# Optimization experiments

Hardware: AMD Instinct MI355X
Metric: run time of the kernel (lower is better)

## Reference

```python
import jax, jax.numpy as jnp
import numpy as np
import math

EMBED_DIM = 256
NUM_HEADS = 8
NUM_LEVELS = 4
NUM_POINTS_LIST = [4, 4, 4, 4]
SUM_P = sum(NUM_POINTS_LIST)            # 16
TOTAL_POINTS = NUM_HEADS * SUM_P        # 128
HEAD_DIM = EMBED_DIM // NUM_HEADS       # 32
OFFSET_SCALE = 0.5
SPATIAL = [(100, 100), (50, 50), (25, 25), (13, 13)]
BS, LQ = 16, 1000
LV = sum(h * w for h, w in SPATIAL)     # 13294
NUM_POINTS_SCALE = np.concatenate([np.full(n, 1.0 / n, np.float32) for n in NUM_POINTS_LIST])


def _grid_init_bias():
    # Faithful to MSDeformableAttention._reset_parameters
    thetas = np.arange(NUM_HEADS, dtype=np.float32) * (2.0 * math.pi / NUM_HEADS)
    grid = np.stack([np.cos(thetas), np.sin(thetas)], -1)          # [H,2]
    grid = grid / np.abs(grid).max(-1, keepdims=True)
    grid = np.tile(grid.reshape(NUM_HEADS, 1, 2), (1, SUM_P, 1))   # [H,SUM_P,2]
    scaling = np.concatenate([np.arange(1, n + 1) for n in NUM_POINTS_LIST]).reshape(1, -1, 1)
    grid = grid * scaling
    return grid.reshape(-1).astype(np.float32)                     # [TOTAL_POINTS*2]


def setup_inputs() -> dict:
    key = jax.random.key(0)
    k1, k2, k3, k4, k5 = jax.random.split(key, 5)
    return {
        "query": jax.random.normal(k1, (BS, LQ, EMBED_DIM), dtype=jnp.float32),
        "reference_points": jax.random.uniform(k2, (BS, LQ, 1, 4), dtype=jnp.float32),
        "value": jax.random.normal(k3, (BS, LV, EMBED_DIM), dtype=jnp.float32),
        "value_spatial_shapes": np.asarray(SPATIAL, dtype=np.int64),
        "W_off": jax.random.normal(k4, (EMBED_DIM, TOTAL_POINTS * 2), dtype=jnp.float32) * 0.01,
        "b_off": jnp.asarray(_grid_init_bias()),
        "W_attn": jax.random.normal(k5, (EMBED_DIM, TOTAL_POINTS), dtype=jnp.float32) * 0.01,
        "b_attn": jnp.zeros((TOTAL_POINTS,), dtype=jnp.float32),
    }


def _bilinear(valf, px, py, H, W):
    # valf: [bs, h, H*W, d]; px, py: [bs, h, n] pixel coords (grid_sample,
    # align_corners=False, padding_mode='zeros' semantics)
    x0 = jnp.floor(px)
    y0 = jnp.floor(py)
    wx1 = px - x0
    wy1 = py - y0
    x0i = x0.astype(jnp.int32)
    y0i = y0.astype(jnp.int32)

    def g(xi, yi):
        valid = ((xi >= 0) & (xi < W) & (yi >= 0) & (yi < H)).astype(valf.dtype)
        idx = jnp.clip(yi, 0, H - 1) * W + jnp.clip(xi, 0, W - 1)
        return jnp.take_along_axis(valf, idx[..., None], axis=2) * valid[..., None]

    return (g(x0i, y0i) * ((1 - wx1) * (1 - wy1))[..., None]
            + g(x0i + 1, y0i) * (wx1 * (1 - wy1))[..., None]
            + g(x0i, y0i + 1) * ((1 - wx1) * wy1)[..., None]
            + g(x0i + 1, y0i + 1) * (wx1 * wy1)[..., None])


def reference(query, reference_points, value, value_spatial_shapes, W_off, b_off, W_attn, b_attn):
    shapes = [(int(h), int(w)) for h, w in np.asarray(value_spatial_shapes)]
    bs, Lq, C = query.shape
    # sampling offsets + attention weights projections
    off = (query @ W_off + b_off).reshape(bs, Lq, NUM_HEADS, SUM_P, 2)
    attn = jax.nn.softmax((query @ W_attn + b_attn).reshape(bs, Lq, NUM_HEADS, SUM_P), axis=-1)
    nps = jnp.asarray(NUM_POINTS_SCALE)
    # reference_points: [bs,Lq,1,4] -> [:, :, None, :, :] broadcasts over heads & points
    offset = off * nps[:, None] * reference_points[:, :, None, :, 2:] * OFFSET_SCALE
    loc = reference_points[:, :, None, :, :2] + offset        # [bs,Lq,H,SUM_P,2]

    value_h = value.reshape(bs, -1, NUM_HEADS, HEAD_DIM).transpose(0, 2, 1, 3)  # [bs,H,Lv,d]
    out = jnp.zeros((bs, NUM_HEADS, Lq, HEAD_DIM), dtype=query.dtype)
    v_start, p_start = 0, 0
    for lvl, (H_, W_) in enumerate(shapes):
        n_l = H_ * W_
        P_l = NUM_POINTS_LIST[lvl]
        valf = value_h[:, :, v_start:v_start + n_l]                    # [bs,H,HW,d]
        loc_l = loc[:, :, :, p_start:p_start + P_l]                    # [bs,Lq,H,P,2]
        loc_l = loc_l.transpose(0, 2, 1, 3, 4).reshape(bs, NUM_HEADS, Lq * P_l, 2)
        # grid_sample align_corners=False: pixel = loc * size - 0.5
        px = loc_l[..., 0] * W_ - 0.5
        py = loc_l[..., 1] * H_ - 0.5
        samp = _bilinear(valf, px, py, H_, W_).reshape(bs, NUM_HEADS, Lq, P_l, HEAD_DIM)
        a_l = attn[:, :, :, p_start:p_start + P_l].transpose(0, 2, 1, 3)  # [bs,H,Lq,P]
        out = out + jnp.einsum('bhqp,bhqpd->bhqd', a_l, samp)
        v_start += n_l
        p_start += P_l
    return out.transpose(0, 2, 1, 3).reshape(bs, Lq, C)
```

## Files before the change

### kernel.cpp

```cpp
#include <hip/hip_runtime.h>


#define BS   16
#define LQ   1000
#define LV   13294
#define CDIM 256
#define NH   8
#define HD   32
#define SP   16
#define NA   (NH*SP)
#define QB   8
#define NBLK ((BS*LQ)/QB)

__global__ __launch_bounds__(256) void msda_fused(
    const float* __restrict__ query,
    const float* __restrict__ refp,
    const float* __restrict__ value,
    const float* __restrict__ Woff,
    const float* __restrict__ boff,
    const float* __restrict__ Wattn,
    const float* __restrict__ battn,
    float* __restrict__ out)
{
    __shared__ float smem[QB*NA + QB*CDIM];
    float (*qlds)[CDIM] = (float (*)[CDIM])smem;
    float (*attn_s)[NA] = (float (*)[NA])smem;
    float (*loc_s)[CDIM] = (float (*)[CDIM])(smem + QB*NA);
    __shared__ float ref_s[QB][4];

    const int t  = threadIdx.x;
    const int q0 = blockIdx.x * QB;

    for (int i = t; i < QB*CDIM; i += 256) {
        qlds[i >> 8][i & 255] = query[(size_t)q0 * CDIM + i];
    }
    if (t < QB*4) {
        ref_s[t >> 2][t & 3] = refp[(size_t)q0 * 4 + t];
    }
    __syncthreads();

    float acc_off[QB];
    float acc_at[QB];
    #pragma unroll
    for (int qq = 0; qq < QB; ++qq) { acc_off[qq] = 0.f; acc_at[qq] = 0.f; }

    const float bo = boff[t];
    const float ba = (t < NA) ? battn[t] : 0.f;

    for (int k4 = 0; k4 < CDIM/4; ++k4) {
        const int k = k4 * 4;
        const float w0 = Woff[(k+0)*CDIM + t];
        const float w1 = Woff[(k+1)*CDIM + t];
        const float w2 = Woff[(k+2)*CDIM + t];
        const float w3 = Woff[(k+3)*CDIM + t];
        #pragma unroll
        for (int qq = 0; qq < QB; ++qq) {
            const float4 qv = *reinterpret_cast<const float4*>(&qlds[qq][k]);
            float a = acc_off[qq];
            a = fmaf(w0, qv.x, a);
            a = fmaf(w1, qv.y, a);
            a = fmaf(w2, qv.z, a);
            a = fmaf(w3, qv.w, a);
            acc_off[qq] = a;
        }
    }
    if (t < NA) {
        for (int k4 = 0; k4 < CDIM/4; ++k4) {
            const int k = k4 * 4;
            const float w0 = Wattn[(k+0)*NA + t];
            const float w1 = Wattn[(k+1)*NA + t];
            const float w2 = Wattn[(k+2)*NA + t];
            const float w3 = Wattn[(k+3)*NA + t];
            #pragma unroll
            for (int qq = 0; qq < QB; ++qq) {
                const float4 qv = *reinterpret_cast<const float4*>(&qlds[qq][k]);
                float a = acc_at[qq];
                a = fmaf(w0, qv.x, a);
                a = fmaf(w1, qv.y, a);
                a = fmaf(w2, qv.z, a);
                a = fmaf(w3, qv.w, a);
                acc_at[qq] = a;
            }
        }
    }

    __syncthreads();

    if (t < NA) {
        #pragma unroll
        for (int qq = 0; qq < QB; ++qq) {
            const float x = acc_at[qq] + ba;
            float m = x;
            #pragma unroll
            for (int d = 1; d < SP; d <<= 1) m = fmaxf(m, __shfl_xor(m, d, 64));
            const float e = __expf(x - m);
            float s = e;
            #pragma unroll
            for (int d = 1; d < SP; d <<= 1) s += __shfl_xor(s, d, 64);
            attn_s[qq][t] = e / s;
        }
    }
    {
        const int cc = t & 1;
        #pragma unroll
        for (int qq = 0; qq < QB; ++qq) {
            const float o   = acc_off[qq] + bo;
            const float r   = ref_s[qq][cc];
            const float rwh = ref_s[qq][2 + cc];
            loc_s[qq][t] = fmaf(o * 0.125f, rwh, r);
        }
    }
    __syncthreads();

    const int sq   = t >> 6;
    const int lane = t & 63;
    const int h    = lane >> 3;
    const int c4   = (lane & 7) << 2;
    const int b    = q0 / LQ;
    const float* __restrict__ vb = value + (size_t)b * LV * CDIM + h*HD + c4;

    const int HWs[4] = {100, 50, 25, 13};
    const int Ss[4]  = {0, 10000, 12500, 13125};

    #pragma unroll 1
    for (int qq0 = 0; qq0 < QB; qq0 += 4) {
        const int qq = qq0 + sq;
        const int qg = q0 + qq;
        float4 acc = {0.f, 0.f, 0.f, 0.f};
        #pragma unroll 4
        for (int p = 0; p < SP; ++p) {
            const int lvl = p >> 2;
            const int Wl = HWs[lvl];
            const int Hl = HWs[lvl];
            const float lx = loc_s[qq][(h*SP + p)*2 + 0];
            const float ly = loc_s[qq][(h*SP + p)*2 + 1];
            const float a  = attn_s[qq][h*SP + p];

            const float px = lx * (float)Wl - 0.5f;
            const float py = ly * (float)Hl - 0.5f;
            const float fx = floorf(px), fy = floorf(py);
            const int   x0 = (int)fx,   y0 = (int)fy;
            const float wx1 = px - fx,  wy1 = py - fy;
            const float wx0 = 1.f - wx1, wy0 = 1.f - wy1;

            const bool xok0 = (x0 >= 0)  && (x0 < Wl);
            const bool xok1 = (x0 >= -1) && (x0+1 < Wl);
            const bool yok0 = (y0 >= 0)  && (y0 < Hl);
            const bool yok1 = (y0 >= -1) && (y0+1 < Hl);

            const int xc0 = min(max(x0,   0), Wl-1);
            const int xc1 = min(max(x0+1, 0), Wl-1);
            const int yc0 = min(max(y0,   0), Hl-1);
            const int yc1 = min(max(y0+1, 0), Hl-1);

            const float w00 = (xok0 && yok0) ? a*wx0*wy0 : 0.f;
            const float w10 = (xok1 && yok0) ? a*wx1*wy0 : 0.f;
            const float w01 = (xok0 && yok1) ? a*wx0*wy1 : 0.f;
            const float w11 = (xok1 && yok1) ? a*wx1*wy1 : 0.f;

            const float* __restrict__ lb = vb + (size_t)Ss[lvl] * CDIM;
            const float4 v00 = *reinterpret_cast<const float4*>(lb + (size_t)(yc0*Wl + xc0) * CDIM);
            const float4 v10 = *reinterpret_cast<const float4*>(lb + (size_t)(yc0*Wl + xc1) * CDIM);
            const float4 v01 = *reinterpret_cast<const float4*>(lb + (size_t)(yc1*Wl + xc0) * CDIM);
            const float4 v11 = *reinterpret_cast<const float4*>(lb + (size_t)(yc1*Wl + xc1) * CDIM);

            acc.x = fmaf(v00.x, w00, fmaf(v10.x, w10, fmaf(v01.x, w01, fmaf(v11.x, w11, acc.x))));
            acc.y = fmaf(v00.y, w00, fmaf(v10.y, w10, fmaf(v01.y, w01, fmaf(v11.y, w11, acc.y))));
            acc.z = fmaf(v00.z, w00, fmaf(v10.z, w10, fmaf(v01.z, w01, fmaf(v11.z, w11, acc.z))));
            acc.w = fmaf(v00.w, w00, fmaf(v10.w, w10, fmaf(v01.w, w01, fmaf(v11.w, w11, acc.w))));
        }
        *reinterpret_cast<float4*>(&out[(size_t)qg * CDIM + h*HD + c4]) = acc;
    }
}

extern "C" void kernel_launch(void* const* d_in, const int* in_sizes, int n_in,
                              void* d_out, int out_size, void* d_ws, size_t ws_size,
                              hipStream_t stream) {
    const float* query = (const float*)d_in[0];
    const float* refp  = (const float*)d_in[1];
    const float* value = (const float*)d_in[2];
    const float* Woff  = (const float*)d_in[4];
    const float* boff  = (const float*)d_in[5];
    const float* Wattn = (const float*)d_in[6];
    const float* battn = (const float*)d_in[7];
    float* outp = (float*)d_out;

    msda_fused<<<NBLK, 256, 0, stream>>>(query, refp, value, Woff, boff, Wattn, battn, outp);
}
```

Measured before the change: 400.5 us.

## Split attention-logit GEMV across all threads and interleave two queries in sampling loop

The attention-weight projection now uses all 256 threads, with each half covering half of the K dimension; partial sums are combined through a new shared-memory buffer. This removes the idle half-block during that phase. The sampling loop now handles two queries per thread in the same point loop instead of two sequential passes, which puts more independent gathers in flight. It also adds a launch-bounds occupancy hint of 3 and uses 32-bit shifted indexing. The costs are extra shared memory and possible register pressure under the occupancy cap.

```diff
diff --git a/kernel.cpp b/kernel.cpp
--- a/kernel.cpp
+++ b/kernel.cpp
@@ -12,7 +12,7 @@
 #define QB   8
 #define NBLK ((BS*LQ)/QB)
 
-__global__ __launch_bounds__(256) void msda_fused(
+__global__ __launch_bounds__(256, 3) void msda_fused(
     const float* __restrict__ query,
     const float* __restrict__ refp,
     const float* __restrict__ value,
@@ -26,6 +26,7 @@
     float (*qlds)[CDIM] = (float (*)[CDIM])smem;
     float (*attn_s)[NA] = (float (*)[NA])smem;
     float (*loc_s)[CDIM] = (float (*)[CDIM])(smem + QB*NA);
+    __shared__ float attn_part[QB][NA][2];
     __shared__ float ref_s[QB][4];
 
     const int t  = threadIdx.x;
@@ -40,12 +41,9 @@
     __syncthreads();
 
     float acc_off[QB];
-    float acc_at[QB];
     #pragma unroll
-    for (int qq = 0; qq < QB; ++qq) { acc_off[qq] = 0.f; acc_at[qq] = 0.f; }
-
+    for (int qq = 0; qq < QB; ++qq) acc_off[qq] = 0.f;
     const float bo = boff[t];
-    const float ba = (t < NA) ? battn[t] : 0.f;
 
     for (int k4 = 0; k4 < CDIM/4; ++k4) {
         const int k = k4 * 4;
@@ -64,13 +62,21 @@
             acc_off[qq] = a;
         }
     }
-    if (t < NA) {
-        for (int k4 = 0; k4 < CDIM/4; ++k4) {
-            const int k = k4 * 4;
-            const float w0 = Wattn[(k+0)*NA + t];
-            const float w1 = Wattn[(k+1)*NA + t];
-            const float w2 = Wattn[(k+2)*NA + t];
-            const float w3 = Wattn[(k+3)*NA + t];
+
+    {
+        const int ac    = t & (NA-1);
+        const int half  = t >> 7;
+        const int kbase = half << 7;
+        float acc_at[QB];
+        #pragma unroll
+        for (int qq = 0; qq < QB; ++qq) acc_at[qq] = 0.f;
+
+        for (int k4 = 0; k4 < 32; ++k4) {
+            const int k = kbase + k4 * 4;
+            const float w0 = Wattn[(k+0)*NA + ac];
+            const float w1 = Wattn[(k+1)*NA + ac];
+            const float w2 = Wattn[(k+2)*NA + ac];
+            const float w3 = Wattn[(k+3)*NA + ac];
             #pragma unroll
             for (int qq = 0; qq < QB; ++qq) {
                 const float4 qv = *reinterpret_cast<const float4*>(&qlds[qq][k]);
@@ -82,14 +88,18 @@
                 acc_at[qq] = a;
             }
         }
+        #pragma unroll
+        for (int qq = 0; qq < QB; ++qq) attn_part[qq][ac][half] = acc_at[qq];
     }
 
     __syncthreads();
 
     if (t < NA) {
+        const float ba = battn[t];
         #pragma unroll
         for (int qq = 0; qq < QB; ++qq) {
-            const float x = acc_at[qq] + ba;
+            const float2 pr = *reinterpret_cast<const float2*>(&attn_part[qq][t][0]);
+            const float x = pr.x + pr.y + ba;
             float m = x;
             #pragma unroll
             for (int d = 1; d < SP; d <<= 1) m = fmaxf(m, __shfl_xor(m, d, 64));
@@ -122,55 +132,63 @@
     const int HWs[4] = {100, 50, 25, 13};
     const int Ss[4]  = {0, 10000, 12500, 13125};
 
-    #pragma unroll 1
-    for (int qq0 = 0; qq0 < QB; qq0 += 4) {
-        const int qq = qq0 + sq;
-        const int qg = q0 + qq;
-        float4 acc = {0.f, 0.f, 0.f, 0.f};
-        #pragma unroll 4
-        for (int p = 0; p < SP; ++p) {
-            const int lvl = p >> 2;
-            const int Wl = HWs[lvl];
-            const int Hl = HWs[lvl];
-            const float lx = loc_s[qq][(h*SP + p)*2 + 0];
-            const float ly = loc_s[qq][(h*SP + p)*2 + 1];
-            const float a  = attn_s[qq][h*SP + p];
-
-            const float px = lx * (float)Wl - 0.5f;
-            const float py = ly * (float)Hl - 0.5f;
-            const float fx = floorf(px), fy = floorf(py);
-            const int   x0 = (int)fx,   y0 = (int)fy;
-            const float wx1 = px - fx,  wy1 = py - fy;
-            const float wx0 = 1.f - wx1, wy0 = 1.f - wy1;
-
-            const bool xok0 = (x0 >= 0)  && (x0 < Wl);
-            const bool xok1 = (x0 >= -1) && (x0+1 < Wl);
-            const bool yok0 = (y0 >= 0)  && (y0 < Hl);
-            const bool yok1 = (y0 >= -1) && (y0+1 < Hl);
-
-            const int xc0 = min(max(x0,   0), Wl-1);
-            const int xc1 = min(max(x0+1, 0), Wl-1);
-            const int yc0 = min(max(y0,   0), Hl-1);
-            const int yc1 = min(max(y0+1, 0), Hl-1);
-
-            const float w00 = (xok0 && yok0) ? a*wx0*wy0 : 0.f;
-            const float w10 = (xok1 && yok0) ? a*wx1*wy0 : 0.f;
-            const float w01 = (xok0 && yok1) ? a*wx0*wy1 : 0.f;
-            const float w11 = (xok1 && yok1) ? a*wx1*wy1 : 0.f;
-
-            const float* __restrict__ lb = vb + (size_t)Ss[lvl] * CDIM;
-            const float4 v00 = *reinterpret_cast<const float4*>(lb + (size_t)(yc0*Wl + xc0) * CDIM);
-            const float4 v10 = *reinterpret_cast<const float4*>(lb + (size_t)(yc0*Wl + xc1) * CDIM);
-            const float4 v01 = *reinterpret_cast<const float4*>(lb + (size_t)(yc1*Wl + xc0) * CDIM);
-            const float4 v11 = *reinterpret_cast<const float4*>(lb + (size_t)(yc1*Wl + xc1) * CDIM);
-
-            acc.x = fmaf(v00.x, w00, fmaf(v10.x, w10, fmaf(v01.x, w01, fmaf(v11.x, w11, acc.x))));
-            acc.y = fmaf(v00.y, w00, fmaf(v10.y, w10, fmaf(v01.y, w01, fmaf(v11.y, w11, acc.y))));
-            acc.z = fmaf(v00.z, w00, fmaf(v10.z, w10, fmaf(v01.z, w01, fmaf(v11.z, w11, acc.z))));
-            acc.w = fmaf(v00.w, w00, fmaf(v10.w, w10, fmaf(v01.w, w01, fmaf(v11.w, w11, acc.w))));
-        }
-        *reinterpret_cast<float4*>(&out[(size_t)qg * CDIM + h*HD + c4]) = acc;
-    }
+    const int qA = sq;
+    const int qB2 = sq + 4;
+    float4 accA = {0.f, 0.f, 0.f, 0.f};
+    float4 accB = {0.f, 0.f, 0.f, 0.f};
+
+    auto tap = [&](int qq, int p, int Wl, int Soff, float4& acc) {
+        const int hp = h*SP + p;
+        const float lx = loc_s[qq][hp*2 + 0];
+        const float ly = loc_s[qq][hp*2 + 1];
+        const float a  = attn_s[qq][hp];
+
+        const float px = fmaf(lx, (float)Wl, -0.5f);
+        const float py = fmaf(ly, (float)Wl, -0.5f);
+        const float fx = floorf(px), fy = floorf(py);
+        const int   x0 = (int)fx,   y0 = (int)fy;
+        const float wx1 = px - fx,  wy1 = py - fy;
+        const float wx0 = 1.f - wx1, wy0 = 1.f - wy1;
+
+        const bool xok0 = (x0 >= 0)  && (x0 < Wl);
+        const bool xok1 = (x0 >= -1) && (x0 < Wl-1);
+        const bool yok0 = (y0 >= 0)  && (y0 < Wl);
+        const bool yok1 = (y0 >= -1) && (y0 < Wl-1);
+
+        const int xc0 = min(max(x0,   0), Wl-1);
+        const int xc1 = min(max(x0+1, 0), Wl-1);
+        const int yc0 = min(max(y0,   0), Wl-1);
+        const int yc1 = min(max(y0+1, 0), Wl-1);
+
+        const float w00 = (xok0 && yok0) ? a*wx0*wy0 : 0.f;
+        const float w10 = (xok1 && yok0) ? a*wx1*wy0 : 0.f;
+        const float w01 = (xok0 && yok1) ? a*wx0*wy1 : 0.f;
+        const float w11 = (xok1 && yok1) ? a*wx1*wy1 : 0.f;
+
+        const int r0 = Soff + yc0*Wl;
+        const int r1 = Soff + yc1*Wl;
+        const float4 v00 = *reinterpret_cast<const float4*>(vb + ((r0 + xc0) << 8));
+        const float4 v10 = *reinterpret_cast<const float4*>(vb + ((r0 + xc1) << 8));
+        const float4 v01 = *reinterpret_cast<const float4*>(vb + ((r1 + xc0) << 8));
+        const float4 v11 = *reinterpret_cast<const float4*>(vb + ((r1 + xc1) << 8));
+
+        acc.x = fmaf(v00.x, w00, fmaf(v10.x, w10, fmaf(v01.x, w01, fmaf(v11.x, w11, acc.x))));
+        acc.y = fmaf(v00.y, w00, fmaf(v10.y, w10, fmaf(v01.y, w01, fmaf(v11.y, w11, acc.y))));
+        acc.z = fmaf(v00.z, w00, fmaf(v10.z, w10, fmaf(v01.z, w01, fmaf(v11.z, w11, acc.z))));
+        acc.w = fmaf(v00.w, w00, fmaf(v10.w, w10, fmaf(v01.w, w01, fmaf(v11.w, w11, acc.w))));
+    };
+
+    #pragma unroll 2
+    for (int p = 0; p < SP; ++p) {
+        const int lvl  = p >> 2;
+        const int Wl   = HWs[lvl];
+        const int Soff = Ss[lvl];
+        tap(qA,  p, Wl, Soff, accA);
+        tap(qB2, p, Wl, Soff, accB);
+    }
+
+    *reinterpret_cast<float4*>(&out[(size_t)(q0 + qA)  * CDIM + h*HD + c4]) = accA;
+    *reinterpret_cast<float4*>(&out[(size_t)(q0 + qB2) * CDIM + h*HD + c4]) = accB;
 }
 
 extern "C" void kernel_launch(void* const* d_in, const int* in_sizes, int n_in,
```

New measurement: 394.1 us. Within noise of the previous version (-1.6%).
